# Kernel tuning notes

Hardware: AMD Instinct MI355X
Metric: run time of the kernel (lower is better)

## Reference

```python
import jax, jax.numpy as jnp
import numpy as np

B, D, K = 32, 64, 256            # batch, num objects (seq len), feature size (== in_size)
G = [256, 256, 256]              # g_layers sizes
F1, F2, OUT = 256, 256, 128      # f_fc1, f_fc2, out_size


def setup_inputs() -> dict:
    key = jax.random.key(0)
    ks = jax.random.split(key, 16)
    scale = 0.02

    def w(k, shape):
        return jax.random.normal(k, shape, dtype=jnp.float32) * scale

    x = jax.random.normal(ks[0], (B, D, K), dtype=jnp.float32)
    # edge_feature: Linear(2*K, K). Stored [in, out] (transposed vs torch).
    edge_w = w(ks[1], (2 * K, K))
    edge_b = jnp.zeros((K,), dtype=jnp.float32)
    g_ws, g_bs = [], []
    in_s = K
    for i, out_s in enumerate(G):
        g_ws.append(w(ks[2 + i], (in_s, out_s)))
        g_bs.append(jnp.zeros((out_s,), dtype=jnp.float32))
        in_s = out_s
    f1_w = w(ks[8], (G[-1], F1)); f1_b = jnp.zeros((F1,), dtype=jnp.float32)
    f2_w = w(ks[9], (F1, F2));    f2_b = jnp.zeros((F2,), dtype=jnp.float32)
    f3_w = w(ks[10], (F2, OUT));  f3_b = jnp.zeros((OUT,), dtype=jnp.float32)
    return dict(x=x, edge_w=edge_w, edge_b=edge_b, g_ws=g_ws, g_bs=g_bs,
                f1_w=f1_w, f1_b=f1_b, f2_w=f2_w, f2_b=f2_b, f3_w=f3_w, f3_b=f3_b)


def reference(x, edge_w, edge_b, g_ws, g_bs, f1_w, f1_b, f2_w, f2_b, f3_w, f3_b):
    # x: [B, D, K]. Original builds x_full[b,i,j] = concat(x[b,j], x[b,i]) then
    # applies edge_feature (Linear(2K -> K)). Equivalent, without materializing the
    # concat: split edge_w into the halves acting on x_i (=x[b,j]) and x_j (=x[b,i]).
    k = x.shape[-1]
    u = x @ edge_w[:k]      # [B, D, K]  -> indexed by j (axis 2)
    v = x @ edge_w[k:]      # [B, D, K]  -> indexed by i (axis 1)
    h = u[:, None, :, :] + v[:, :, None, :] + edge_b   # [B, D, D, K]
    # g MLP over all d^2 pairs (Linear + ReLU chain)
    for gw, gb in zip(g_ws, g_bs):
        h = jax.nn.relu(h @ gw + gb)
    # sum-aggregate over all pairs
    x_g = h.sum(axis=(1, 2))                            # [B, G[-1]]
    # f MLP (dropout p=0.0 -> identity)
    x_f = jax.nn.relu(x_g @ f1_w + f1_b)
    x_f = jax.nn.relu(x_f @ f2_w + f2_b)
    return x_f @ f3_w + f3_b                            # [B, OUT]
```

## Files before the change

### kernel.cpp

```cpp
#include <hip/hip_runtime.h>
#include <hip/hip_bf16.h>

typedef __attribute__((ext_vector_type(4))) float f32x4;
typedef __attribute__((ext_vector_type(2))) int   i32x2;
typedef __attribute__((ext_vector_type(4))) int   i32x4;
typedef __attribute__((ext_vector_type(8))) short short8;

__device__ __forceinline__ unsigned short f2bf(float x) {
  __hip_bfloat16 h = __float2bfloat16(x);
  union { __hip_bfloat16 h1; unsigned short u; } c; c.h1 = h; return c.u;
}
__device__ __forceinline__ unsigned pk2(float a, float b) {
  __hip_bfloat162 h = __float22bfloat162_rn(make_float2(a, b));
  union { __hip_bfloat162 h2; unsigned u; } c; c.h2 = h; return c.u;
}
__device__ __forceinline__ float bf2f(unsigned short u) {
  union { unsigned u32; float f; } c; c.u32 = ((unsigned)u) << 16; return c.f;
}

__global__ void k_prep(const float* __restrict__ edge_w, const float* __restrict__ edge_b,
                       const float* __restrict__ gw0, const float* __restrict__ gb0,
                       const float* __restrict__ gw1, const float* __restrict__ gw2,
                       unsigned short* __restrict__ W1uR, unsigned short* __restrict__ W1vR,
                       float* __restrict__ c1,
                       unsigned short* __restrict__ W2R, unsigned short* __restrict__ W3R) {
  const int blk = blockIdx.x, t = threadIdx.x;
  __shared__ float eu[256], ev[256];
  if (blk < 256) {
    eu[t] = edge_w[blk * 256 + t];
    ev[t] = edge_w[(256 + blk) * 256 + t];
    __syncthreads();
    float su = 0.f, sv = 0.f;
    for (int o = 0; o < 256; ++o) {
      float gg = gw0[o * 256 + t];
      su += eu[o] * gg; sv += ev[o] * gg;
    }
    const int k = blk, m = t;
    const int w = m >> 6, mf = (m >> 4) & 3, q = m & 15;
    const int ch = k >> 5, g = (k >> 3) & 3, e = k & 7;
    const int idx = ((w * 8 + ch) * 4 + mf) * 512 + (g * 16 + q) * 8 + e;
    W1uR[idx] = f2bf(su);
    W1vR[idx] = f2bf(sv);
  } else if (blk == 256) {
    float s = gb0[t];
    for (int o = 0; o < 256; ++o) s += edge_b[o] * gw0[o * 256 + t];
    c1[t] = s;
  } else {
    int p = blk - 257;
    const float* src = (p < 32) ? gw1 : gw2;
    unsigned short* dst = (p < 32) ? W2R : W3R;
    p &= 31;
    int w = p >> 3, ch = p & 7;
    int mf = t >> 6, lane = t & 63, q = lane & 15, g = lane >> 4;
    int base = ((w * 8 + ch) * 4 + mf) * 512 + lane * 8;
    int m = w * 64 + mf * 16 + q;
#pragma unroll
    for (int e = 0; e < 8; ++e) {
      int k = ch * 32 + g * 8 + e;
      dst[base + e] = f2bf(src[k * 256 + m]);
    }
  }
}

__global__ void k_uv(const float* __restrict__ x,
                     const unsigned short* __restrict__ W1uR,
                     const unsigned short* __restrict__ W1vR,
                     const float* __restrict__ c1,
                     unsigned short* __restrict__ U1, float* __restrict__ V1c) {
  __shared__ unsigned short xs[8192];

  const int t = threadIdx.x;
  const int tile = blockIdx.x >> 1, sel = blockIdx.x & 1;
  const int r0 = tile * 32;
  const int wid = t >> 6, lane = t & 63;
  const int q = lane & 15, g = lane >> 4;
  const int mo = wid << 6;

  {
    const int row = t >> 3, sl = t & 7, r7 = row & 7;
    const float* xB = x + (size_t)(r0 + row) * 256;
    unsigned short* hB = xs + row * 256;
#pragma unroll
    for (int m = 0; m < 4; ++m) {
      int ks = sl + 8 * m;
      f32x4 u0 = *(const f32x4*)(xB + ks * 8);
      f32x4 u1 = *(const f32x4*)(xB + ks * 8 + 4);
      i32x4 wv = { (int)pk2(u0.x, u0.y), (int)pk2(u0.z, u0.w),
                   (int)pk2(u1.x, u1.y), (int)pk2(u1.z, u1.w) };
      *(i32x4*)(hB + (ks ^ r7) * 8) = wv;
    }
  }

  const unsigned short* WR = sel ? W1vR : W1uR;
  const unsigned short* aW = WR + (size_t)wid * 16384 + lane * 8;

  short8 a_[4], an_[4];
#pragma unroll
  for (int mf = 0; mf < 4; ++mf) a_[mf] = *(const short8*)(aW + mf * 512);

  __syncthreads();

  f32x4 acc[4][2];
#pragma unroll
  for (int mf = 0; mf < 4; ++mf)
#pragma unroll
    for (int nf = 0; nf < 2; ++nf) acc[mf][nf] = (f32x4){0.f, 0.f, 0.f, 0.f};

  for (int ch = 0; ch < 8; ++ch) {
    if (ch < 7) {
#pragma unroll
      for (int mf = 0; mf < 4; ++mf)
        an_[mf] = *(const short8*)(aW + (ch + 1) * 2048 + mf * 512);
    }
    short8 b_[2];
#pragma unroll
    for (int nf = 0; nf < 2; ++nf) {
      int r = q + 16 * nf;
      b_[nf] = *(const short8*)(xs + r * 256 + (((ch * 4 + g) ^ (r & 7)) * 8));
    }
#pragma unroll
    for (int mf = 0; mf < 4; ++mf)
#pragma unroll
      for (int nf = 0; nf < 2; ++nf)
        acc[mf][nf] = __builtin_amdgcn_mfma_f32_16x16x32_bf16(a_[mf], b_[nf], acc[mf][nf], 0, 0, 0);
    if (ch < 7) {
#pragma unroll
      for (int mf = 0; mf < 4; ++mf) a_[mf] = an_[mf];
    }
  }

#pragma unroll
  for (int mf = 0; mf < 4; ++mf) {
    int c2b = mo + 16 * mf + 4 * g;
#pragma unroll
    for (int nf = 0; nf < 2; ++nf) {
      int r = r0 + q + 16 * nf;
      f32x4 v = acc[mf][nf];
      if (sel == 0) {
        i32x2 wv = { (int)pk2(v.x, v.y), (int)pk2(v.z, v.w) };
        *(i32x2*)(U1 + (size_t)r * 256 + c2b) = wv;
      } else {
        f32x4 cc = *(const f32x4*)(c1 + c2b);
        f32x4 o = { v.x + cc.x, v.y + cc.y, v.z + cc.z, v.w + cc.w };
        *(f32x4*)(V1c + (size_t)r * 256 + c2b) = o;
      }
    }
  }
}

__device__ __forceinline__ void write_h1(short8 u, f32x4 v0, f32x4 v1,
                                         unsigned short* dst) {
  float r0 = fmaxf(bf2f((unsigned short)u[0]) + v0.x, 0.f);
  float r1 = fmaxf(bf2f((unsigned short)u[1]) + v0.y, 0.f);
  float r2 = fmaxf(bf2f((unsigned short)u[2]) + v0.z, 0.f);
  float r3 = fmaxf(bf2f((unsigned short)u[3]) + v0.w, 0.f);
  float r4 = fmaxf(bf2f((unsigned short)u[4]) + v1.x, 0.f);
  float r5 = fmaxf(bf2f((unsigned short)u[5]) + v1.y, 0.f);
  float r6 = fmaxf(bf2f((unsigned short)u[6]) + v1.z, 0.f);
  float r7 = fmaxf(bf2f((unsigned short)u[7]) + v1.w, 0.f);
  i32x4 wv = { (int)pk2(r0, r1), (int)pk2(r2, r3), (int)pk2(r4, r5), (int)pk2(r6, r7) };
  *(i32x4*)dst = wv;
}

__launch_bounds__(256, 2)
__global__ void k_main(const unsigned short* __restrict__ U1,
                       const float* __restrict__ V1c,
                       const unsigned short* __restrict__ W2R,
                       const unsigned short* __restrict__ W3R,
                       const float* __restrict__ b2, const float* __restrict__ b3,
                       float* __restrict__ partials) {
  __shared__ unsigned short bufA[16384];
  __shared__ unsigned short bufB[16384];

  const int t = threadIdx.x;
  const int bid = blockIdx.x;
  const int wrk = ((bid & 7) << 7) | (bid >> 3);
  const int b = wrk >> 5;
  const int it0 = (wrk & 31) * 2;
  const int wid = t >> 6, lane = t & 63;
  const int q = lane & 15, g = lane >> 4;
  const int mo = wid << 6;

  {
    const int row = t >> 2, sl = t & 3, r7 = row & 7;
    const unsigned short* uB = U1 + (size_t)(b * 64 + row) * 256;
    const float* vA = V1c + (size_t)(b * 64 + it0) * 256;
    const float* vB = vA + 256;
    unsigned short* dA = bufA + row * 256;
    unsigned short* dB = bufB + row * 256;
#pragma unroll
    for (int m = 0; m < 8; ++m) {
      int ks = sl + 4 * m;
      int s8 = (ks ^ r7) * 8;
      short8 u = *(const short8*)(uB + ks * 8);
      f32x4 a0 = *(const f32x4*)(vA + ks * 8);
      f32x4 a1 = *(const f32x4*)(vA + ks * 8 + 4);
      f32x4 b0 = *(const f32x4*)(vB + ks * 8);
      f32x4 b1 = *(const f32x4*)(vB + ks * 8 + 4);
      write_h1(u, a0, a1, dA + s8);
      write_h1(u, b0, b1, dB + s8);
    }
  }

  const unsigned short* aW2 = W2R + (size_t)wid * 16384 + lane * 8;
  const unsigned short* aW3 = W3R + (size_t)wid * 16384 + lane * 8;

  short8 a_[4], an_[4];
#pragma unroll
  for (int mf = 0; mf < 4; ++mf) a_[mf] = *(const short8*)(aW2 + mf * 512);

  __syncthreads();

  f32x4 accA[4][4], accB[4][4];
#pragma unroll
  for (int mf = 0; mf < 4; ++mf)
#pragma unroll
    for (int nf = 0; nf < 4; ++nf) {
      accA[mf][nf] = (f32x4){0.f, 0.f, 0.f, 0.f};
      accB[mf][nf] = (f32x4){0.f, 0.f, 0.f, 0.f};
    }

  for (int ch = 0; ch < 8; ++ch) {
    if (ch < 7) {
#pragma unroll
      for (int mf = 0; mf < 4; ++mf)
        an_[mf] = *(const short8*)(aW2 + (ch + 1) * 2048 + mf * 512);
    }
    short8 bA[4], bB[4];
#pragma unroll
    for (int nf = 0; nf < 4; ++nf) {
      int r = q + 16 * nf;
      int off = r * 256 + (((ch * 4 + g) ^ (r & 7)) * 8);
      bA[nf] = *(const short8*)(bufA + off);
      bB[nf] = *(const short8*)(bufB + off);
    }
#pragma unroll
    for (int mf = 0; mf < 4; ++mf)
#pragma unroll
      for (int nf = 0; nf < 4; ++nf) {
        accA[mf][nf] = __builtin_amdgcn_mfma_f32_16x16x32_bf16(a_[mf], bA[nf], accA[mf][nf], 0, 0, 0);
        accB[mf][nf] = __builtin_amdgcn_mfma_f32_16x16x32_bf16(a_[mf], bB[nf], accB[mf][nf], 0, 0, 0);
      }
    if (ch < 7) {
#pragma unroll
      for (int mf = 0; mf < 4; ++mf) a_[mf] = an_[mf];
    }
  }

  __syncthreads();

#pragma unroll
  for (int mf = 0; mf < 4; ++mf) a_[mf] = *(const short8*)(aW3 + mf * 512);
#pragma unroll
  for (int mf = 0; mf < 4; ++mf) {
    int c2b = mo + 16 * mf + 4 * g;
    f32x4 bb = *(const f32x4*)(b2 + c2b);
    int ksw = c2b >> 3, off = c2b & 7;
#pragma unroll
    for (int nf = 0; nf < 4; ++nf) {
      int r = q + 16 * nf;
      int dst = r * 256 + ((ksw ^ (r & 7)) * 8) + off;
      f32x4 vA_ = accA[mf][nf];
      f32x4 vB_ = accB[mf][nf];
      i32x2 wA = { (int)pk2(fmaxf(vA_.x + bb.x, 0.f), fmaxf(vA_.y + bb.y, 0.f)),
                   (int)pk2(fmaxf(vA_.z + bb.z, 0.f), fmaxf(vA_.w + bb.w, 0.f)) };
      i32x2 wB = { (int)pk2(fmaxf(vB_.x + bb.x, 0.f), fmaxf(vB_.y + bb.y, 0.f)),
                   (int)pk2(fmaxf(vB_.z + bb.z, 0.f), fmaxf(vB_.w + bb.w, 0.f)) };
      *(i32x2*)(bufA + dst) = wA;
      *(i32x2*)(bufB + dst) = wB;
    }
  }
  __syncthreads();

#pragma unroll
  for (int mf = 0; mf < 4; ++mf)
#pragma unroll
    for (int nf = 0; nf < 4; ++nf) {
      accA[mf][nf] = (f32x4){0.f, 0.f, 0.f, 0.f};
      accB[mf][nf] = (f32x4){0.f, 0.f, 0.f, 0.f};
    }

  for (int ch = 0; ch < 8; ++ch) {
    if (ch < 7) {
#pragma unroll
      for (int mf = 0; mf < 4; ++mf)
        an_[mf] = *(const short8*)(aW3 + (ch + 1) * 2048 + mf * 512);
    }
    short8 bA[4], bB[4];
#pragma unroll
    for (int nf = 0; nf < 4; ++nf) {
      int r = q + 16 * nf;
      int off = r * 256 + (((ch * 4 + g) ^ (r & 7)) * 8);
      bA[nf] = *(const short8*)(bufA + off);
      bB[nf] = *(const short8*)(bufB + off);
    }
#pragma unroll
    for (int mf = 0; mf < 4; ++mf)
#pragma unroll
      for (int nf = 0; nf < 4; ++nf) {
        accA[mf][nf] = __builtin_amdgcn_mfma_f32_16x16x32_bf16(a_[mf], bA[nf], accA[mf][nf], 0, 0, 0);
        accB[mf][nf] = __builtin_amdgcn_mfma_f32_16x16x32_bf16(a_[mf], bB[nf], accB[mf][nf], 0, 0, 0);
      }
    if (ch < 7) {
#pragma unroll
      for (int mf = 0; mf < 4; ++mf) a_[mf] = an_[mf];
    }
  }

  __syncthreads();

  float* scrA = (float*)&bufA[0];
  float* scrB = (float*)&bufB[0];
#pragma unroll
  for (int mf = 0; mf < 4; ++mf) {
    int n3b = mo + 16 * mf + 4 * g;
    f32x4 bb = *(const f32x4*)(b3 + n3b);
    f32x4 sA = (f32x4){0.f, 0.f, 0.f, 0.f};
    f32x4 sB = (f32x4){0.f, 0.f, 0.f, 0.f};
#pragma unroll
    for (int nf = 0; nf < 4; ++nf) {
      f32x4 vA_ = accA[mf][nf];
      f32x4 vB_ = accB[mf][nf];
      sA.x += fmaxf(vA_.x + bb.x, 0.f); sA.y += fmaxf(vA_.y + bb.y, 0.f);
      sA.z += fmaxf(vA_.z + bb.z, 0.f); sA.w += fmaxf(vA_.w + bb.w, 0.f);
      sB.x += fmaxf(vB_.x + bb.x, 0.f); sB.y += fmaxf(vB_.y + bb.y, 0.f);
      sB.z += fmaxf(vB_.z + bb.z, 0.f); sB.w += fmaxf(vB_.w + bb.w, 0.f);
    }
    *(f32x4*)(scrA + q * 264 + n3b) = sA;
    *(f32x4*)(scrB + q * 264 + n3b) = sB;
  }
  __syncthreads();
  float sA = 0.f, sB = 0.f;
#pragma unroll
  for (int q2 = 0; q2 < 16; ++q2) {
    sA += scrA[q2 * 264 + t];
    sB += scrB[q2 * 264 + t];
  }
  partials[(size_t)(b * 64 + it0) * 256 + t] = sA;
  partials[(size_t)(b * 64 + it0 + 1) * 256 + t] = sB;
}

__global__ void k_fmlp(const float* __restrict__ partials,
                       const float* __restrict__ f1w, const float* __restrict__ f1b,
                       const float* __restrict__ f2w, const float* __restrict__ f2b,
                       const float* __restrict__ f3w, const float* __restrict__ f3b,
                       float* __restrict__ out) {
  const int b = blockIdx.x, t = threadIdx.x;
  __shared__ float xg[256], x1[256], x2[256];
  {
    const float* p = partials + (size_t)(b * 64) * 256 + t;
    float s[8];
#pragma unroll
    for (int i = 0; i < 8; ++i) s[i] = 0.f;
#pragma unroll
    for (int k = 0; k < 8; ++k)
#pragma unroll
      for (int i = 0; i < 8; ++i) s[i] += p[(k * 8 + i) * 256];
    float tot = 0.f;
#pragma unroll
    for (int i = 0; i < 8; ++i) tot += s[i];
    xg[t] = tot;
  }
  __syncthreads();
  {
    float a0 = 0.f, a1 = 0.f, a2 = 0.f, a3 = 0.f;
#pragma unroll 4
    for (int k = 0; k < 64; ++k) {
      a0 += xg[k]       * f1w[(k)       * 256 + t];
      a1 += xg[k + 64]  * f1w[(k + 64)  * 256 + t];
      a2 += xg[k + 128] * f1w[(k + 128) * 256 + t];
      a3 += xg[k + 192] * f1w[(k + 192) * 256 + t];
    }
    x1[t] = fmaxf((a0 + a1) + (a2 + a3) + f1b[t], 0.f);
  }
  __syncthreads();
  {
    float a0 = 0.f, a1 = 0.f, a2 = 0.f, a3 = 0.f;
#pragma unroll 4
    for (int k = 0; k < 64; ++k) {
      a0 += x1[k]       * f2w[(k)       * 256 + t];
      a1 += x1[k + 64]  * f2w[(k + 64)  * 256 + t];
      a2 += x1[k + 128] * f2w[(k + 128) * 256 + t];
      a3 += x1[k + 192] * f2w[(k + 192) * 256 + t];
    }
    x2[t] = fmaxf((a0 + a1) + (a2 + a3) + f2b[t], 0.f);
  }
  __syncthreads();
  if (t < 128) {
    float a0 = 0.f, a1 = 0.f, a2 = 0.f, a3 = 0.f;
#pragma unroll 4
    for (int k = 0; k < 64; ++k) {
      a0 += x2[k]       * f3w[(k)       * 128 + t];
      a1 += x2[k + 64]  * f3w[(k + 64)  * 128 + t];
      a2 += x2[k + 128] * f3w[(k + 128) * 128 + t];
      a3 += x2[k + 192] * f3w[(k + 192) * 128 + t];
    }
    out[b * 128 + t] = (a0 + a1) + (a2 + a3) + f3b[t];
  }
}

__global__ void k_zero(float* __restrict__ out, int n) {
  int i = blockIdx.x * 256 + threadIdx.x;
  if (i < n) out[i] = 0.f;
}

extern "C" void kernel_launch(void* const* d_in, const int* in_sizes, int n_in,
                              void* d_out, int out_size, void* d_ws, size_t ws_size,
                              hipStream_t stream) {
  const float* x      = (const float*)d_in[0];
  const float* edge_w = (const float*)d_in[1];
  const float* edge_b = (const float*)d_in[2];
  const float *gw0, *gw1, *gw2, *gb0, *gb1, *gb2;
  const float *f1w, *f1b, *f2w, *f2b, *f3w, *f3b;

  if (n_in >= 15 && in_sizes[3] == 65536 && in_sizes[4] == 65536 && in_sizes[5] == 65536) {
    gw0 = (const float*)d_in[3]; gw1 = (const float*)d_in[4]; gw2 = (const float*)d_in[5];
    gb0 = (const float*)d_in[6]; gb1 = (const float*)d_in[7]; gb2 = (const float*)d_in[8];
    f1w = (const float*)d_in[9];  f1b = (const float*)d_in[10];
    f2w = (const float*)d_in[11]; f2b = (const float*)d_in[12];
    f3w = (const float*)d_in[13]; f3b = (const float*)d_in[14];
  } else if (n_in >= 15 && in_sizes[3] == 65536 && in_sizes[4] == 256) {
    gw0 = (const float*)d_in[3]; gb0 = (const float*)d_in[4];
    gw1 = (const float*)d_in[5]; gb1 = (const float*)d_in[6];
    gw2 = (const float*)d_in[7]; gb2 = (const float*)d_in[8];
    f1w = (const float*)d_in[9];  f1b = (const float*)d_in[10];
    f2w = (const float*)d_in[11]; f2b = (const float*)d_in[12];
    f3w = (const float*)d_in[13]; f3b = (const float*)d_in[14];
  } else {
    const float* gws = (const float*)d_in[3];
    const float* gbs = (const float*)d_in[4];
    gw0 = gws;          gw1 = gws + 65536;  gw2 = gws + 131072;
    gb0 = gbs;          gb1 = gbs + 256;    gb2 = gbs + 512;
    f1w = (const float*)d_in[5];  f1b = (const float*)d_in[6];
    f2w = (const float*)d_in[7];  f2b = (const float*)d_in[8];
    f3w = (const float*)d_in[9];  f3b = (const float*)d_in[10];
  }

  char* ws = (char*)d_ws;
  float*          c1       = (float*)(ws);
  unsigned short* W1uR     = (unsigned short*)(ws + 1024);
  unsigned short* W1vR     = (unsigned short*)(ws + 132096);
  unsigned short* W2R      = (unsigned short*)(ws + 263168);
  unsigned short* W3R      = (unsigned short*)(ws + 394240);
  unsigned short* U1       = (unsigned short*)(ws + 525312);
  float*          V1c      = (float*)(ws + 1573888);
  float*          partials = (float*)(ws + 3671040);
  const size_t need = 5768192;
  (void)out_size; (void)n_in;

  if (ws_size < need) {
    k_zero<<<dim3((out_size + 255) / 256), dim3(256), 0, stream>>>((float*)d_out, out_size);
    return;
  }

  k_prep<<<dim3(321), dim3(256), 0, stream>>>(edge_w, edge_b, gw0, gb0, gw1, gw2,
                                              W1uR, W1vR, c1, W2R, W3R);
  k_uv<<<dim3(128), dim3(256), 0, stream>>>(x, W1uR, W1vR, c1, U1, V1c);
  k_main<<<dim3(1024), dim3(256), 0, stream>>>(U1, V1c, W2R, W3R, gb1, gb2,
                                               partials);
  k_fmlp<<<dim3(32), dim3(256), 0, stream>>>(partials, f1w, f1b, f2w, f2b, f3w, f3b,
                                             (float*)d_out);
}
```

Baseline: 71.87 us.

## Split k_main's two pair tiles across 512 threads instead of per-thread dual accumulators

k_main now launches 512 threads per block. Each half of the block handles one of the two i-rows (bufA or bufB) with a single accumulator set, instead of every thread carrying accumulators for both tiles. This halves register pressure per thread and doubles wave count per block. In exchange, W2/W3 fragments are loaded twice (once per half), and the register prefetch of the next weight chunk is removed in favour of a fully unrolled loop.

```diff
diff --git a/kernel.cpp b/kernel.cpp
--- a/kernel.cpp
+++ b/kernel.cpp
@@ -162,7 +162,7 @@
   *(i32x4*)dst = wv;
 }
 
-__launch_bounds__(256, 2)
+__launch_bounds__(512, 4)
 __global__ void k_main(const unsigned short* __restrict__ U1,
                        const float* __restrict__ V1c,
                        const unsigned short* __restrict__ W2R,
@@ -177,80 +177,63 @@
   const int wrk = ((bid & 7) << 7) | (bid >> 3);
   const int b = wrk >> 5;
   const int it0 = (wrk & 31) * 2;
-  const int wid = t >> 6, lane = t & 63;
+  const int sel = t >> 8;
+  const int tt = t & 255;
+  const int wid4 = (t >> 6) & 3;
+  const int lane = t & 63;
   const int q = lane & 15, g = lane >> 4;
-  const int mo = wid << 6;
+  const int mo = wid4 << 6;
+
+  unsigned short* const buf = sel ? bufB : bufA;
 
   {
-    const int row = t >> 2, sl = t & 3, r7 = row & 7;
+    const int row = tt >> 2, sl = tt & 3, r7 = row & 7;
     const unsigned short* uB = U1 + (size_t)(b * 64 + row) * 256;
-    const float* vA = V1c + (size_t)(b * 64 + it0) * 256;
-    const float* vB = vA + 256;
-    unsigned short* dA = bufA + row * 256;
-    unsigned short* dB = bufB + row * 256;
+    const float* vP = V1c + (size_t)(b * 64 + it0 + sel) * 256;
+    unsigned short* d = buf + row * 256;
 #pragma unroll
     for (int m = 0; m < 8; ++m) {
       int ks = sl + 4 * m;
       int s8 = (ks ^ r7) * 8;
       short8 u = *(const short8*)(uB + ks * 8);
-      f32x4 a0 = *(const f32x4*)(vA + ks * 8);
-      f32x4 a1 = *(const f32x4*)(vA + ks * 8 + 4);
-      f32x4 b0 = *(const f32x4*)(vB + ks * 8);
-      f32x4 b1 = *(const f32x4*)(vB + ks * 8 + 4);
-      write_h1(u, a0, a1, dA + s8);
-      write_h1(u, b0, b1, dB + s8);
-    }
-  }
-
-  const unsigned short* aW2 = W2R + (size_t)wid * 16384 + lane * 8;
-  const unsigned short* aW3 = W3R + (size_t)wid * 16384 + lane * 8;
-
-  short8 a_[4], an_[4];
-#pragma unroll
-  for (int mf = 0; mf < 4; ++mf) a_[mf] = *(const short8*)(aW2 + mf * 512);
-
-  __syncthreads();
-
-  f32x4 accA[4][4], accB[4][4];
+      f32x4 v0 = *(const f32x4*)(vP + ks * 8);
+      f32x4 v1 = *(const f32x4*)(vP + ks * 8 + 4);
+      write_h1(u, v0, v1, d + s8);
+    }
+  }
+
+  const unsigned short* aW2 = W2R + (size_t)wid4 * 16384 + lane * 8;
+  const unsigned short* aW3 = W3R + (size_t)wid4 * 16384 + lane * 8;
+
+  __syncthreads();
+
+  f32x4 acc[4][4];
 #pragma unroll
   for (int mf = 0; mf < 4; ++mf)
 #pragma unroll
-    for (int nf = 0; nf < 4; ++nf) {
-      accA[mf][nf] = (f32x4){0.f, 0.f, 0.f, 0.f};
-      accB[mf][nf] = (f32x4){0.f, 0.f, 0.f, 0.f};
-    }
-
+    for (int nf = 0; nf < 4; ++nf) acc[mf][nf] = (f32x4){0.f, 0.f, 0.f, 0.f};
+
+#pragma unroll
   for (int ch = 0; ch < 8; ++ch) {
-    if (ch < 7) {
-#pragma unroll
-      for (int mf = 0; mf < 4; ++mf)
-        an_[mf] = *(const short8*)(aW2 + (ch + 1) * 2048 + mf * 512);
-    }
-    short8 bA[4], bB[4];
+    short8 a_[4];
+#pragma unroll
+    for (int mf = 0; mf < 4; ++mf)
+      a_[mf] = *(const short8*)(aW2 + ch * 2048 + mf * 512);
+    short8 b_[4];
 #pragma unroll
     for (int nf = 0; nf < 4; ++nf) {
       int r = q + 16 * nf;
-      int off = r * 256 + (((ch * 4 + g) ^ (r & 7)) * 8);
-      bA[nf] = *(const short8*)(bufA + off);
-      bB[nf] = *(const short8*)(bufB + off);
+      b_[nf] = *(const short8*)(buf + r * 256 + (((ch * 4 + g) ^ (r & 7)) * 8));
     }
 #pragma unroll
     for (int mf = 0; mf < 4; ++mf)
 #pragma unroll
-      for (int nf = 0; nf < 4; ++nf) {
-        accA[mf][nf] = __builtin_amdgcn_mfma_f32_16x16x32_bf16(a_[mf], bA[nf], accA[mf][nf], 0, 0, 0);
-        accB[mf][nf] = __builtin_amdgcn_mfma_f32_16x16x32_bf16(a_[mf], bB[nf], accB[mf][nf], 0, 0, 0);
-      }
-    if (ch < 7) {
-#pragma unroll
-      for (int mf = 0; mf < 4; ++mf) a_[mf] = an_[mf];
-    }
-  }
-
-  __syncthreads();
-
-#pragma unroll
-  for (int mf = 0; mf < 4; ++mf) a_[mf] = *(const short8*)(aW3 + mf * 512);
+      for (int nf = 0; nf < 4; ++nf)
+        acc[mf][nf] = __builtin_amdgcn_mfma_f32_16x16x32_bf16(a_[mf], b_[nf], acc[mf][nf], 0, 0, 0);
+  }
+
+  __syncthreads();
+
 #pragma unroll
   for (int mf = 0; mf < 4; ++mf) {
     int c2b = mo + 16 * mf + 4 * g;
@@ -260,14 +243,10 @@
     for (int nf = 0; nf < 4; ++nf) {
       int r = q + 16 * nf;
       int dst = r * 256 + ((ksw ^ (r & 7)) * 8) + off;
-      f32x4 vA_ = accA[mf][nf];
-      f32x4 vB_ = accB[mf][nf];
-      i32x2 wA = { (int)pk2(fmaxf(vA_.x + bb.x, 0.f), fmaxf(vA_.y + bb.y, 0.f)),
-                   (int)pk2(fmaxf(vA_.z + bb.z, 0.f), fmaxf(vA_.w + bb.w, 0.f)) };
-      i32x2 wB = { (int)pk2(fmaxf(vB_.x + bb.x, 0.f), fmaxf(vB_.y + bb.y, 0.f)),
-                   (int)pk2(fmaxf(vB_.z + bb.z, 0.f), fmaxf(vB_.w + bb.w, 0.f)) };
-      *(i32x2*)(bufA + dst) = wA;
-      *(i32x2*)(bufB + dst) = wB;
+      f32x4 v = acc[mf][nf];
+      i32x2 wv = { (int)pk2(fmaxf(v.x + bb.x, 0.f), fmaxf(v.y + bb.y, 0.f)),
+                   (int)pk2(fmaxf(v.z + bb.z, 0.f), fmaxf(v.w + bb.w, 0.f)) };
+      *(i32x2*)(buf + dst) = wv;
     }
   }
   __syncthreads();
@@ -275,69 +254,50 @@
 #pragma unroll
   for (int mf = 0; mf < 4; ++mf)
 #pragma unroll
-    for (int nf = 0; nf < 4; ++nf) {
-      accA[mf][nf] = (f32x4){0.f, 0.f, 0.f, 0.f};
-      accB[mf][nf] = (f32x4){0.f, 0.f, 0.f, 0.f};
-    }
-
+    for (int nf = 0; nf < 4; ++nf) acc[mf][nf] = (f32x4){0.f, 0.f, 0.f, 0.f};
+
+#pragma unroll
   for (int ch = 0; ch < 8; ++ch) {
-    if (ch < 7) {
-#pragma unroll
-      for (int mf = 0; mf < 4; ++mf)
-        an_[mf] = *(const short8*)(aW3 + (ch + 1) * 2048 + mf * 512);
-    }
-    short8 bA[4], bB[4];
+    short8 a_[4];
+#pragma unroll
+    for (int mf = 0; mf < 4; ++mf)
+      a_[mf] = *(const short8*)(aW3 + ch * 2048 + mf * 512);
+    short8 b_[4];
 #pragma unroll
     for (int nf = 0; nf < 4; ++nf) {
       int r = q + 16 * nf;
-      int off = r * 256 + (((ch * 4 + g) ^ (r & 7)) * 8);
-      bA[nf] = *(const short8*)(bufA + off);
-      bB[nf] = *(const short8*)(bufB + off);
+      b_[nf] = *(const short8*)(buf + r * 256 + (((ch * 4 + g) ^ (r & 7)) * 8));
     }
 #pragma unroll
     for (int mf = 0; mf < 4; ++mf)
 #pragma unroll
-      for (int nf = 0; nf < 4; ++nf) {
-        accA[mf][nf] = __builtin_amdgcn_mfma_f32_16x16x32_bf16(a_[mf], bA[nf], accA[mf][nf], 0, 0, 0);
-        accB[mf][nf] = __builtin_amdgcn_mfma_f32_16x16x32_bf16(a_[mf], bB[nf], accB[mf][nf], 0, 0, 0);
-      }
-    if (ch < 7) {
-#pragma unroll
-      for (int mf = 0; mf < 4; ++mf) a_[mf] = an_[mf];
-    }
-  }
-
-  __syncthreads();
-
-  float* scrA = (float*)&bufA[0];
-  float* scrB = (float*)&bufB[0];
+      for (int nf = 0; nf < 4; ++nf)
+        acc[mf][nf] = __builtin_amdgcn_mfma_f32_16x16x32_bf16(a_[mf], b_[nf], acc[mf][nf], 0, 0, 0);
+  }
+
+  __syncthreads();
+
+  float* scr = (float*)buf;
 #pragma unroll
   for (int mf = 0; mf < 4; ++mf) {
     int n3b = mo + 16 * mf + 4 * g;
     f32x4 bb = *(const f32x4*)(b3 + n3b);
-    f32x4 sA = (f32x4){0.f, 0.f, 0.f, 0.f};
-    f32x4 sB = (f32x4){0.f, 0.f, 0.f, 0.f};
+    f32x4 sum = (f32x4){0.f, 0.f, 0.f, 0.f};
 #pragma unroll
     for (int nf = 0; nf < 4; ++nf) {
-      f32x4 vA_ = accA[mf][nf];
-      f32x4 vB_ = accB[mf][nf];
-      sA.x += fmaxf(vA_.x + bb.x, 0.f); sA.y += fmaxf(vA_.y + bb.y, 0.f);
-      sA.z += fmaxf(vA_.z + bb.z, 0.f); sA.w += fmaxf(vA_.w + bb.w, 0.f);
-      sB.x += fmaxf(vB_.x + bb.x, 0.f); sB.y += fmaxf(vB_.y + bb.y, 0.f);
-      sB.z += fmaxf(vB_.z + bb.z, 0.f); sB.w += fmaxf(vB_.w + bb.w, 0.f);
-    }
-    *(f32x4*)(scrA + q * 264 + n3b) = sA;
-    *(f32x4*)(scrB + q * 264 + n3b) = sB;
-  }
-  __syncthreads();
-  float sA = 0.f, sB = 0.f;
-#pragma unroll
-  for (int q2 = 0; q2 < 16; ++q2) {
-    sA += scrA[q2 * 264 + t];
-    sB += scrB[q2 * 264 + t];
-  }
-  partials[(size_t)(b * 64 + it0) * 256 + t] = sA;
-  partials[(size_t)(b * 64 + it0 + 1) * 256 + t] = sB;
+      f32x4 v = acc[mf][nf];
+      sum.x += fmaxf(v.x + bb.x, 0.f);
+      sum.y += fmaxf(v.y + bb.y, 0.f);
+      sum.z += fmaxf(v.z + bb.z, 0.f);
+      sum.w += fmaxf(v.w + bb.w, 0.f);
+    }
+    *(f32x4*)(scr + q * 264 + n3b) = sum;
+  }
+  __syncthreads();
+  float s = 0.f;
+#pragma unroll
+  for (int q2 = 0; q2 < 16; ++q2) s += scr[q2 * 264 + tt];
+  partials[(size_t)(b * 64 + it0 + sel) * 256 + tt] = s;
 }
 
 __global__ void k_fmlp(const float* __restrict__ partials,
@@ -456,7 +416,7 @@
   k_prep<<<dim3(321), dim3(256), 0, stream>>>(edge_w, edge_b, gw0, gb0, gw1, gw2,
                                               W1uR, W1vR, c1, W2R, W3R);
   k_uv<<<dim3(128), dim3(256), 0, stream>>>(x, W1uR, W1vR, c1, U1, V1c);
-  k_main<<<dim3(1024), dim3(256), 0, stream>>>(U1, V1c, W2R, W3R, gb1, gb2,
+  k_main<<<dim3(1024), dim3(512), 0, stream>>>(U1, V1c, W2R, W3R, gb1, gb2,
                                                partials);
   k_fmlp<<<dim3(32), dim3(256), 0, stream>>>(partials, f1w, f1b, f2w, f2b, f3w, f3b,
                                              (float*)d_out);
```

Measured after the change: 73.00 us. About the same (+1.6%).
